# Optimization experiments

Measured on AMD Instinct MI355X. Metric: run time of the kernel, lower is better.

Reference implementation:

```python
import jax, jax.numpy as jnp
import numpy as np

EPS = 1e-6
NUM_HEADS = 16
CAPACITY_FACTOR = 0.5


def _layernorm(x, g, b):
    mu = jnp.mean(x, axis=-1, keepdims=True)
    var = jnp.mean((x - mu) ** 2, axis=-1, keepdims=True)
    return (x - mu) * jax.lax.rsqrt(var + EPS) * g + b


def setup_inputs() -> dict:
    key = jax.random.key(0)
    ks = jax.random.split(key, 12)
    B, S, H, F = 2, 2048, 1024, 4096
    s = lambda d: 1.0 / np.sqrt(d)
    return {
        "x": jax.random.normal(ks[0], (B, S, H), jnp.float32),
        "w_router": jax.random.normal(ks[1], (1, H), jnp.float32) * s(H),
        "ln1_g": jnp.ones((H,), jnp.float32),
        "ln1_b": jnp.zeros((H,), jnp.float32),
        "wq": jax.random.normal(ks[2], (H, H), jnp.float32) * s(H),
        "wk": jax.random.normal(ks[3], (H, H), jnp.float32) * s(H),
        "wv": jax.random.normal(ks[4], (H, H), jnp.float32) * s(H),
        "wo": jax.random.normal(ks[5], (H, H), jnp.float32) * s(H),
        "ln2_g": jnp.ones((H,), jnp.float32),
        "ln2_b": jnp.zeros((H,), jnp.float32),
        "w_gate": jax.random.normal(ks[6], (F, H), jnp.float32) * s(H),
        "w_up": jax.random.normal(ks[7], (F, H), jnp.float32) * s(H),
        "w_down": jax.random.normal(ks[8], (H, F), jnp.float32) * s(F),
    }


def reference(x, w_router, ln1_g, ln1_b, wq, wk, wv, wo, ln2_g, ln2_b, w_gate, w_up, w_down):
    B, S, H = x.shape
    nh = NUM_HEADS
    hd = H // nh
    scale = hd ** -0.5

    # --- TokenRouter (training path, straight-through) ---
    router_logits = jnp.einsum("bsh,oh->bso", x, w_router)[..., 0]  # [B,S]
    capacity = int(S * CAPACITY_FACTOR)
    _, top_idx = jax.lax.top_k(router_logits, capacity)  # [B,cap]
    routing_mask = jnp.zeros((B, S), x.dtype).at[jnp.arange(B)[:, None], top_idx].set(1.0)
    probs = jax.nn.sigmoid(router_logits)
    routing_weights = (routing_mask + probs - jax.lax.stop_gradient(probs))[..., None]  # [B,S,1]

    # --- Attention sub-block ---
    residual = x
    xn = _layernorm(x, ln1_g, ln1_b)
    q = jnp.einsum("bsh,oh->bso", xn, wq).reshape(B, S, nh, hd).transpose(0, 2, 1, 3)
    k = jnp.einsum("bsh,oh->bso", xn, wk).reshape(B, S, nh, hd).transpose(0, 2, 1, 3)
    v = jnp.einsum("bsh,oh->bso", xn, wv).reshape(B, S, nh, hd).transpose(0, 2, 1, 3)
    scores = jnp.einsum("bnqd,bnkd->bnqk", q, k) * scale
    causal = jnp.triu(jnp.full((S, S), -jnp.inf, x.dtype), k=1)
    attn = jax.nn.softmax(scores + causal, axis=-1)
    out = jnp.einsum("bnqk,bnkd->bnqd", attn, v).transpose(0, 2, 1, 3).reshape(B, S, H)
    attn_out = jnp.einsum("bsh,oh->bso", out, wo)
    x = residual + routing_weights * attn_out

    # --- FFN sub-block (SwiGLU) ---
    residual = x
    xn = _layernorm(x, ln2_g, ln2_b)
    gate = jax.nn.silu(jnp.einsum("bsh,fh->bsf", xn, w_gate))
    up = jnp.einsum("bsh,fh->bsf", xn, w_up)
    ffn_out = jnp.einsum("bsf,hf->bsh", gate * up, w_down)
    x = residual + routing_weights * ffn_out

    return x, router_logits
```

## Files before the change

### kernel.cpp

```cpp
#include <hip/hip_runtime.h>
#include <hip/hip_bf16.h>

typedef unsigned short u16;
typedef __attribute__((ext_vector_type(4))) float f32x4;
typedef __attribute__((ext_vector_type(8))) short short8;
typedef __attribute__((ext_vector_type(4))) unsigned short ushort4v;

__device__ __forceinline__ u16 f2bfu(float f) {
  unsigned int u = __float_as_uint(f);
  u += 0x7FFFu + ((u >> 16) & 1u);
  return (u16)(u >> 16);
}
__device__ __forceinline__ f32x4 mfma16(short8 a, short8 b, f32x4 c) {
  return __builtin_amdgcn_mfma_f32_16x16x32_bf16(a, b, c, 0, 0, 0);
}
__device__ __forceinline__ void gld16(const void* g, void* l) {
  __builtin_amdgcn_global_load_lds(
      (const __attribute__((address_space(1))) void*)g,
      (__attribute__((address_space(3))) void*)l, 16, 0, 0);
}

__global__ void k_cvt7(const float* __restrict__ s0, const float* __restrict__ s1,
                       const float* __restrict__ s2, const float* __restrict__ s3,
                       const float* __restrict__ s4, const float* __restrict__ s5,
                       const float* __restrict__ s6,
                       u16* __restrict__ d0, u16* __restrict__ d1, u16* __restrict__ d2,
                       u16* __restrict__ d3, u16* __restrict__ d4, u16* __restrict__ d5,
                       u16* __restrict__ d6) {
  const int y = blockIdx.y;
  const float* src; u16* dst; int n4;
  switch (y) {
    case 0: src = s0; dst = d0; n4 = 262144; break;
    case 1: src = s1; dst = d1; n4 = 262144; break;
    case 2: src = s2; dst = d2; n4 = 262144; break;
    case 3: src = s3; dst = d3; n4 = 262144; break;
    case 4: src = s4; dst = d4; n4 = 1048576; break;
    case 5: src = s5; dst = d5; n4 = 1048576; break;
    default: src = s6; dst = d6; n4 = 1048576; break;
  }
  int i = blockIdx.x * blockDim.x + threadIdx.x;
  if (i < n4) {
    float4 v = ((const float4*)src)[i];
    ushort4v o;
    o.x = f2bfu(v.x); o.y = f2bfu(v.y); o.z = f2bfu(v.z); o.w = f2bfu(v.w);
    *(ushort4v*)(dst + (size_t)i * 4) = o;
  }
}

__global__ void k_router(const float* __restrict__ x, const float* __restrict__ wr,
                         float* __restrict__ logits, float* __restrict__ out_lg,
                         float* __restrict__ out_x) {
  int t = blockIdx.x * 4 + (threadIdx.x >> 6);
  int l = threadIdx.x & 63;
  const float* xp = x + (size_t)t * 1024;
  float* op = out_x + (size_t)t * 1024;
  float s = 0.f;
#pragma unroll
  for (int p = 0; p < 4; ++p) {
    float4 xv = *(const float4*)(xp + (p * 64 + l) * 4);
    float4 wv = *(const float4*)(wr + (p * 64 + l) * 4);
    s += xv.x * wv.x + xv.y * wv.y + xv.z * wv.z + xv.w * wv.w;
    *(float4*)(op + (p * 64 + l) * 4) = xv;
  }
#pragma unroll
  for (int off = 32; off; off >>= 1) s += __shfl_xor(s, off);
  if (l == 0) { logits[t] = s; out_lg[t] = s; }
}

__global__ void k_mask(const float* __restrict__ logits, float* __restrict__ mask) {
  __shared__ float lg[2048];
  int b = blockIdx.y;
  const float* lp = logits + b * 2048;
  for (int j = threadIdx.x; j < 2048; j += 256) lg[j] = lp[j];
  __syncthreads();
  int t = threadIdx.x >> 2, qtr = threadIdx.x & 3;
  int i = blockIdx.x * 64 + t;
  float my = lg[i];
  int cnt = 0;
  for (int j = qtr * 512; j < qtr * 512 + 512; j += 4) {
    float4 v = *(const float4*)&lg[j];
    cnt += (v.x > my) || (v.x == my && (j + 0) < i);
    cnt += (v.y > my) || (v.y == my && (j + 1) < i);
    cnt += (v.z > my) || (v.z == my && (j + 2) < i);
    cnt += (v.w > my) || (v.w == my && (j + 3) < i);
  }
  cnt += __shfl_xor(cnt, 1);
  cnt += __shfl_xor(cnt, 2);
  if (qtr == 0) mask[b * 2048 + i] = (cnt < 1024) ? 1.0f : 0.0f;
}

__global__ void k_scan(const float* __restrict__ mask, int* __restrict__ idx) {
  __shared__ int wsum[4];
  int b = blockIdx.x;
  const float* mp = mask + b * 2048;
  int t = threadIdx.x, lane = t & 63, wv = t >> 6;
  int sel[8]; int c = 0;
#pragma unroll
  for (int j = 0; j < 8; ++j) { sel[j] = mp[t * 8 + j] > 0.5f; c += sel[j]; }
  int sc = c;
#pragma unroll
  for (int off = 1; off < 64; off <<= 1) {
    int u = __shfl_up(sc, off);
    if (lane >= off) sc += u;
  }
  if (lane == 63) wsum[wv] = sc;
  __syncthreads();
  int woff = 0;
  for (int i = 0; i < wv; ++i) woff += wsum[i];
  int pos = woff + sc - c;
#pragma unroll
  for (int j = 0; j < 8; ++j)
    if (sel[j]) idx[b * 1024 + pos++] = t * 8 + j;
}

__global__ void k_ln(const float* __restrict__ x, const float* __restrict__ g,
                     const float* __restrict__ bb, u16* __restrict__ out) {
  int t = blockIdx.x * 4 + (threadIdx.x >> 6);
  int l = threadIdx.x & 63;
  const float* xp = x + (size_t)t * 1024;
  float4 xv[4];
  float s = 0.f, sq = 0.f;
#pragma unroll
  for (int p = 0; p < 4; ++p) {
    xv[p] = *(const float4*)(xp + (p * 64 + l) * 4);
    s += xv[p].x + xv[p].y + xv[p].z + xv[p].w;
    sq += xv[p].x * xv[p].x + xv[p].y * xv[p].y + xv[p].z * xv[p].z + xv[p].w * xv[p].w;
  }
#pragma unroll
  for (int off = 32; off; off >>= 1) { s += __shfl_xor(s, off); sq += __shfl_xor(sq, off); }
  float mu = s * (1.f / 1024.f);
  float var = sq * (1.f / 1024.f) - mu * mu;
  float rs = rsqrtf(var + 1e-6f);
#pragma unroll
  for (int p = 0; p < 4; ++p) {
    float4 gv = *(const float4*)(g + (p * 64 + l) * 4);
    float4 bv = *(const float4*)(bb + (p * 64 + l) * 4);
    ushort4v o;
    o.x = f2bfu((xv[p].x - mu) * rs * gv.x + bv.x);
    o.y = f2bfu((xv[p].y - mu) * rs * gv.y + bv.y);
    o.z = f2bfu((xv[p].z - mu) * rs * gv.z + bv.z);
    o.w = f2bfu((xv[p].w - mu) * rs * gv.w + bv.w);
    *(ushort4v*)(out + (size_t)t * 1024 + (p * 64 + l) * 4) = o;
  }
}

__global__ void k_ln_g(const float* __restrict__ x, const int* __restrict__ idx,
                       const float* __restrict__ g, const float* __restrict__ bb,
                       u16* __restrict__ out) {
  int t = blockIdx.x * 4 + (threadIdx.x >> 6);
  int l = threadIdx.x & 63;
  int b = t >> 10;
  int orig = idx[b * 1024 + (t & 1023)];
  const float* xp = x + ((size_t)(b * 2048 + orig)) * 1024;
  float4 xv[4];
  float s = 0.f, sq = 0.f;
#pragma unroll
  for (int p = 0; p < 4; ++p) {
    xv[p] = *(const float4*)(xp + (p * 64 + l) * 4);
    s += xv[p].x + xv[p].y + xv[p].z + xv[p].w;
    sq += xv[p].x * xv[p].x + xv[p].y * xv[p].y + xv[p].z * xv[p].z + xv[p].w * xv[p].w;
  }
#pragma unroll
  for (int off = 32; off; off >>= 1) { s += __shfl_xor(s, off); sq += __shfl_xor(sq, off); }
  float mu = s * (1.f / 1024.f);
  float var = sq * (1.f / 1024.f) - mu * mu;
  float rs = rsqrtf(var + 1e-6f);
#pragma unroll
  for (int p = 0; p < 4; ++p) {
    float4 gv = *(const float4*)(g + (p * 64 + l) * 4);
    float4 bv = *(const float4*)(bb + (p * 64 + l) * 4);
    ushort4v o;
    o.x = f2bfu((xv[p].x - mu) * rs * gv.x + bv.x);
    o.y = f2bfu((xv[p].y - mu) * rs * gv.y + bv.y);
    o.z = f2bfu((xv[p].z - mu) * rs * gv.z + bv.z);
    o.w = f2bfu((xv[p].w - mu) * rs * gv.w + bv.w);
    *(ushort4v*)(out + (size_t)t * 1024 + (p * 64 + l) * 4) = o;
  }
}

__global__ void k_vtrans(const u16* __restrict__ V, u16* __restrict__ VT) {
  int bh = blockIdx.y;
  int b = bh >> 4, h = bh & 15;
  int w = threadIdx.x >> 6, l = threadIdx.x & 63;
  int s0 = (blockIdx.x * 4 + w) * 32;
  const u16* vb = V + ((size_t)b * 2048) * 1024 + h * 64 + l;
  u16 vals[32];
#pragma unroll
  for (int j = 0; j < 32; ++j) vals[j] = vb[(size_t)(s0 + j) * 1024];
  u16* ob = VT + ((size_t)bh * 64 + l) * 2048 + s0;
#pragma unroll
  for (int c = 0; c < 4; ++c) {
    short8 o;
#pragma unroll
    for (int j = 0; j < 8; ++j) o[j] = (short)vals[c * 8 + j];
    *(short8*)&ob[c * 8] = o;
  }
}

__device__ __forceinline__ void gemm_core64(
    const u16* __restrict__ A, const u16* __restrict__ W,
    u16 (&Al)[2][128][64], u16 (&Bl)[2][128][64],
    int m0, int n0, int K, int k0, int nsteps, f32x4 (&acc)[4][4]) {
  const int tid = threadIdx.x, w = tid >> 6, l = tid & 63;
  const int wr = (w >> 1) * 64, wc = (w & 1) * 64;
#pragma unroll
  for (int mt = 0; mt < 4; ++mt)
#pragma unroll
    for (int nt = 0; nt < 4; ++nt) acc[mt][nt] = (f32x4){0.f, 0.f, 0.f, 0.f};

  auto stage = [&](int bf, int t) {
#pragma unroll
    for (int i = 0; i < 4; ++i) {
      const int bc = (i * 4 + w) * 64;
      const int chunk = bc + l;
      const int row = chunk >> 3, cc = chunk & 7;
      gld16(A + (size_t)(m0 + row) * K + k0 + t * 64 + cc * 8, (char*)(&Al[bf][0][0]) + bc * 16);
      gld16(W + (size_t)(n0 + row) * K + k0 + t * 64 + cc * 8, (char*)(&Bl[bf][0][0]) + bc * 16);
    }
  };

  stage(0, 0);
  for (int t = 0; t < nsteps; ++t) {
    __syncthreads();
    if (t + 1 < nsteps) stage((t + 1) & 1, t + 1);
    const int bf = t & 1;
#pragma unroll
    for (int kk = 0; kk < 2; ++kk) {
      const int ko = kk * 32 + (l >> 4) * 8;
      short8 af[4], bv[4];
#pragma unroll
      for (int mt = 0; mt < 4; ++mt) af[mt] = *(const short8*)&Al[bf][wr + mt * 16 + (l & 15)][ko];
#pragma unroll
      for (int nt = 0; nt < 4; ++nt) bv[nt] = *(const short8*)&Bl[bf][wc + nt * 16 + (l & 15)][ko];
#pragma unroll
      for (int mt = 0; mt < 4; ++mt)
#pragma unroll
        for (int nt = 0; nt < 4; ++nt)
          acc[mt][nt] = mfma16(af[mt], bv[nt], acc[mt][nt]);
    }
  }
}

__global__ __launch_bounds__(256, 2)
void k_qkv(const u16* __restrict__ A,
           const u16* __restrict__ W0, const u16* __restrict__ W1, const u16* __restrict__ W2,
           u16* __restrict__ O0, u16* __restrict__ O1, u16* __restrict__ O2, int K) {
  __shared__ alignas(16) u16 Al[2][128][64];
  __shared__ alignas(16) u16 Bl[2][128][64];
  const int b = blockIdx.x, xcd = b & 7, k = b >> 3;
  const int rowg = xcd * 4 + k / 24, col = k % 24;
  const int sel = col >> 3;
  const u16* W = sel == 0 ? W0 : (sel == 1 ? W1 : W2);
  u16* Ot = sel == 0 ? O0 : (sel == 1 ? O1 : O2);
  const int n0 = (col & 7) * 128, m0 = rowg * 128;
  f32x4 acc[4][4];
  gemm_core64(A, W, Al, Bl, m0, n0, K, 0, K >> 6, acc);
  const int tid = threadIdx.x, w = tid >> 6, l = tid & 63;
  const int wr = (w >> 1) * 64, wc = (w & 1) * 64;
#pragma unroll
  for (int mt = 0; mt < 4; ++mt)
#pragma unroll
    for (int nt = 0; nt < 4; ++nt) {
      int row = m0 + wr + mt * 16 + ((l >> 4) << 2);
      int colo = n0 + wc + nt * 16 + (l & 15);
#pragma unroll
      for (int r = 0; r < 4; ++r)
        Ot[(size_t)(row + r) * 1024 + colo] = f2bfu(acc[mt][nt][r]);
    }
}

__global__ __launch_bounds__(256, 2)
void k_projsk(const u16* __restrict__ A, const u16* __restrict__ W,
              float* __restrict__ P0, float* __restrict__ P1,
              float* __restrict__ P2, float* __restrict__ P3,
              int K, int slice) {
  __shared__ alignas(16) u16 Al[2][128][64];
  __shared__ alignas(16) u16 Bl[2][128][64];
  const int b = blockIdx.x, xcd = b & 7, k = b >> 3;
  const int pair = xcd * 8 + (k >> 3);
  const int rowg = pair >> 2, z = pair & 3, col = k & 7;
  const int n0 = col * 128, m0 = rowg * 128, k0 = z * slice;
  float* P = z == 0 ? P0 : (z == 1 ? P1 : (z == 2 ? P2 : P3));
  f32x4 acc[4][4];
  gemm_core64(A, W, Al, Bl, m0, n0, K, k0, slice >> 6, acc);
  const int tid = threadIdx.x, w = tid >> 6, l = tid & 63;
  const int wr = (w >> 1) * 64, wc = (w & 1) * 64;
#pragma unroll
  for (int mt = 0; mt < 4; ++mt)
#pragma unroll
    for (int nt = 0; nt < 4; ++nt) {
      int row = m0 + wr + mt * 16 + ((l >> 4) << 2);
      int colo = n0 + wc + nt * 16 + (l & 15);
#pragma unroll
      for (int r = 0; r < 4; ++r)
        P[(size_t)(row + r) * 1024 + colo] = acc[mt][nt][r];
    }
}

__global__ void k_combine(const float* __restrict__ P0, const float* __restrict__ P1,
                          const float* __restrict__ P2, const float* __restrict__ P3,
                          const int* __restrict__ idx, const float* __restrict__ resid,
                          float* __restrict__ out) {
  int slot = blockIdx.x * 2 + (threadIdx.x >> 7);
  int c0 = (threadIdx.x & 127) * 8;
  int b = slot >> 10;
  int orig = idx[b * 1024 + (slot & 1023)];
  size_t po = (size_t)slot * 1024 + c0;
  size_t go = ((size_t)(b * 2048 + orig)) * 1024 + c0;
#pragma unroll
  for (int h = 0; h < 2; ++h) {
    float4 a = *(const float4*)(P0 + po + h * 4);
    float4 bb = *(const float4*)(P1 + po + h * 4);
    float4 c = *(const float4*)(P2 + po + h * 4);
    float4 d = *(const float4*)(P3 + po + h * 4);
    float4 rr = *(const float4*)(resid + go + h * 4);
    float4 o;
    o.x = rr.x + a.x + bb.x + c.x + d.x;
    o.y = rr.y + a.y + bb.y + c.y + d.y;
    o.z = rr.z + a.z + bb.z + c.z + d.z;
    o.w = rr.w + a.w + bb.w + c.w + d.w;
    *(float4*)(out + go + h * 4) = o;
  }
}

__global__ __launch_bounds__(256, 2)
void k_ffn_dual(const u16* __restrict__ A, const u16* __restrict__ Wg, const u16* __restrict__ Wu,
                u16* __restrict__ H, int N, int K) {
  __shared__ alignas(16) u16 Al[2][128][32];
  __shared__ alignas(16) u16 Bgl[2][128][32];
  __shared__ alignas(16) u16 Bul[2][128][32];
  const int tid = threadIdx.x, w = tid >> 6, l = tid & 63;
  const int b = blockIdx.x, xcd = b & 7, k = b >> 3;
  const int rowg = xcd * 2 + (k >> 5), col = k & 31;
  const int n0 = col * 128, m0 = rowg * 128;
  const int wr = (w >> 1) * 64, wc = (w & 1) * 64;
  f32x4 ag[4][4], au[4][4];
#pragma unroll
  for (int mt = 0; mt < 4; ++mt)
#pragma unroll
    for (int nt = 0; nt < 4; ++nt) {
      ag[mt][nt] = (f32x4){0.f, 0.f, 0.f, 0.f};
      au[mt][nt] = (f32x4){0.f, 0.f, 0.f, 0.f};
    }
  const int nsteps = K >> 5;

  auto stage = [&](int bf, int t) {
#pragma unroll
    for (int i = 0; i < 2; ++i) {
      const int bc = (i * 4 + w) * 64;
      const int chunk = bc + l;
      const int row = chunk >> 2, cc = chunk & 3;
      const size_t ao = (size_t)(m0 + row) * K + t * 32 + cc * 8;
      const size_t bo = (size_t)(n0 + row) * K + t * 32 + cc * 8;
      gld16(A + ao,  (char*)(&Al[bf][0][0])  + bc * 16);
      gld16(Wg + bo, (char*)(&Bgl[bf][0][0]) + bc * 16);
      gld16(Wu + bo, (char*)(&Bul[bf][0][0]) + bc * 16);
    }
  };

  stage(0, 0);
  for (int t = 0; t < nsteps; ++t) {
    __syncthreads();
    if (t + 1 < nsteps) stage((t + 1) & 1, t + 1);
    const int bf = t & 1;
    const int ko = (l >> 4) * 8;
    short8 af[4], bg[4], bu[4];
#pragma unroll
    for (int mt = 0; mt < 4; ++mt) af[mt] = *(const short8*)&Al[bf][wr + mt * 16 + (l & 15)][ko];
#pragma unroll
    for (int nt = 0; nt < 4; ++nt) {
      bg[nt] = *(const short8*)&Bgl[bf][wc + nt * 16 + (l & 15)][ko];
      bu[nt] = *(const short8*)&Bul[bf][wc + nt * 16 + (l & 15)][ko];
    }
#pragma unroll
    for (int mt = 0; mt < 4; ++mt)
#pragma unroll
      for (int nt = 0; nt < 4; ++nt) {
        ag[mt][nt] = mfma16(af[mt], bg[nt], ag[mt][nt]);
        au[mt][nt] = mfma16(af[mt], bu[nt], au[mt][nt]);
      }
  }
#pragma unroll
  for (int mt = 0; mt < 4; ++mt)
#pragma unroll
    for (int nt = 0; nt < 4; ++nt) {
      int row = m0 + wr + mt * 16 + ((l >> 4) << 2);
      int col2 = n0 + wc + nt * 16 + (l & 15);
#pragma unroll
      for (int r = 0; r < 4; ++r) {
        float g = ag[mt][nt][r], u = au[mt][nt][r];
        float sg = g / (1.f + __expf(-g));
        H[(size_t)(row + r) * N + col2] = f2bfu(sg * u);
      }
    }
}

__global__ __launch_bounds__(512, 4)
void k_attn(const u16* __restrict__ Q, const u16* __restrict__ K,
            const u16* __restrict__ VT, const int* __restrict__ idx,
            u16* __restrict__ O) {
  const int S = 2048, HH = 1024;
  const int px = blockIdx.x, bh = blockIdx.y;
  const int b = bh >> 4, h = bh & 15;
  const int tid = threadIdx.x;
  const int g = tid >> 8;
  const int tg = tid & 255;
  const int w = tg >> 6;
  const int l = tid & 63;
  __shared__ alignas(16) u16 Kl[2][64][72];
  __shared__ alignas(16) u16 Vtl[2][64][72];
  __shared__ alignas(16) u16 Pl[8][16][72];
  __shared__ alignas(16) float cm[4][64][24];
  const size_t base = ((size_t)b * S) * HH + h * 64;
  const u16* vtb = VT + ((size_t)bh * 64) * S;
  const int* ib = idx + b * 1024;

  const int r0 = tg >> 3,          cc0 = (tg & 7) * 8;
  const int r1 = (256 + tg) >> 3,  cc1 = (tg & 7) * 8;

  auto flash = [&](int qt) {
    const int slot0 = qt * 64 + w * 16 + ((l >> 4) << 2);
    const int slotA = qt * 64 + w * 16 + (l & 15);
    const int qrowA = ib[slotA];
    int qp[4];
#pragma unroll
    for (int r = 0; r < 4; ++r) qp[r] = ib[slot0 + r];
    const int nkt = (ib[qt * 64 + 63] >> 6) + 1;
    const int hh = (nkt + 1) >> 1;
    const int kt_base = g ? hh : 0;
    const int kt_end  = g ? nkt : hh;

    short8 qf[2];
#pragma unroll
    for (int kk = 0; kk < 2; ++kk)
      qf[kk] = *(const short8*)&Q[base + (size_t)qrowA * HH + kk * 32 + (l >> 4) * 8];

    f32x4 accO[4];
    float m[4], ls[4];
#pragma unroll
    for (int dt = 0; dt < 4; ++dt) accO[dt] = (f32x4){0.f, 0.f, 0.f, 0.f};
#pragma unroll
    for (int r = 0; r < 4; ++r) { m[r] = -1e30f; ls[r] = 0.f; }

    short8 kreg0, kreg1, vreg0, vreg1;
    auto loadregs = [&](int kt) {
      kreg0 = *(const short8*)&K[base + (size_t)(kt * 64 + r0) * HH + cc0];
      kreg1 = *(const short8*)&K[base + (size_t)(kt * 64 + r1) * HH + cc1];
      vreg0 = *(const short8*)&vtb[(size_t)r0 * S + kt * 64 + cc0];
      vreg1 = *(const short8*)&vtb[(size_t)r1 * S + kt * 64 + cc1];
    };
    if (kt_base < kt_end) loadregs(kt_base);

    for (int i = 0; i < hh; ++i) {
      const int kt = kt_base + i;
      const bool valid = kt < kt_end;
      __syncthreads();
      if (valid) {
        *(short8*)&Kl[g][r0][cc0]  = kreg0;
        *(short8*)&Kl[g][r1][cc1]  = kreg1;
        *(short8*)&Vtl[g][r0][cc0] = vreg0;
        *(short8*)&Vtl[g][r1][cc1] = vreg1;
        if (kt + 1 < kt_end) loadregs(kt + 1);
      }
      __syncthreads();
      if (!valid) continue;

      float p[4][4];
      const int kcb = kt * 64 + (l & 15);
#pragma unroll
      for (int ct = 0; ct < 4; ++ct) {
        f32x4 a = (f32x4){0.f, 0.f, 0.f, 0.f};
#pragma unroll
        for (int kk = 0; kk < 2; ++kk) {
          short8 kf = *(const short8*)&Kl[g][ct * 16 + (l & 15)][kk * 32 + (l >> 4) * 8];
          a = mfma16(qf[kk], kf, a);
        }
#pragma unroll
        for (int r = 0; r < 4; ++r) {
          float v = a[r] * 0.125f;
          if ((kcb + ct * 16) > qp[r]) v = -1e30f;
          p[ct][r] = v;
        }
      }
#pragma unroll
      for (int r = 0; r < 4; ++r) {
        float mx = fmaxf(fmaxf(p[0][r], p[1][r]), fmaxf(p[2][r], p[3][r]));
#pragma unroll
        for (int off = 1; off < 16; off <<= 1) mx = fmaxf(mx, __shfl_xor(mx, off));
        float mn = fmaxf(m[r], mx);
        float alpha = __expf(m[r] - mn);
        m[r] = mn;
        float ps = 0.f;
#pragma unroll
        for (int ct = 0; ct < 4; ++ct) { float e = __expf(p[ct][r] - mn); p[ct][r] = e; ps += e; }
#pragma unroll
        for (int off = 1; off < 16; off <<= 1) ps += __shfl_xor(ps, off);
        ls[r] = ls[r] * alpha + ps;
#pragma unroll
        for (int dt = 0; dt < 4; ++dt) accO[dt][r] *= alpha;
      }
#pragma unroll
      for (int ct = 0; ct < 4; ++ct)
#pragma unroll
        for (int r = 0; r < 4; ++r)
          Pl[g * 4 + w][((l >> 4) << 2) + r][ct * 16 + (l & 15)] = f2bfu(p[ct][r]);
      short8 pa[2];
#pragma unroll
      for (int kk = 0; kk < 2; ++kk)
        pa[kk] = *(const short8*)&Pl[g * 4 + w][l & 15][kk * 32 + (l >> 4) * 8];
#pragma unroll
      for (int dt = 0; dt < 4; ++dt)
#pragma unroll
        for (int kk = 0; kk < 2; ++kk) {
          short8 vf = *(const short8*)&Vtl[g][dt * 16 + (l & 15)][kk * 32 + (l >> 4) * 8];
          accO[dt] = mfma16(pa[kk], vf, accO[dt]);
        }
    }

    __syncthreads();
    if (g == 1) {
      float* dst = &cm[w][l][0];
#pragma unroll
      for (int r = 0; r < 4; ++r) { dst[r] = m[r]; dst[4 + r] = ls[r]; }
#pragma unroll
      for (int dt = 0; dt < 4; ++dt)
#pragma unroll
        for (int r = 0; r < 4; ++r) dst[8 + dt * 4 + r] = accO[dt][r];
    }
    __syncthreads();
    if (g == 0) {
      const float* src = &cm[w][l][0];
#pragma unroll
      for (int r = 0; r < 4; ++r) {
        float m1 = src[r], ls1 = src[4 + r];
        float mm = fmaxf(m[r], m1);
        float a0 = __expf(m[r] - mm), a1 = __expf(m1 - mm);
        float lsf = ls[r] * a0 + ls1 * a1;
        float inv = 1.f / lsf;
#pragma unroll
        for (int dt = 0; dt < 4; ++dt) {
          float v = (accO[dt][r] * a0 + src[8 + dt * 4 + r] * a1) * inv;
          O[((size_t)(b * 1024 + slot0 + r)) * HH + h * 64 + dt * 16 + (l & 15)] = f2bfu(v);
        }
      }
    }
  };

  flash(px);
  flash(15 - px);
}

extern "C" void kernel_launch(void* const* d_in, const int* in_sizes, int n_in,
                              void* d_out, int out_size, void* d_ws, size_t ws_size,
                              hipStream_t stream) {
  const float* x  = (const float*)d_in[0];
  const float* wr = (const float*)d_in[1];
  const float* g1 = (const float*)d_in[2];
  const float* b1 = (const float*)d_in[3];
  const float* wq = (const float*)d_in[4];
  const float* wk = (const float*)d_in[5];
  const float* wv = (const float*)d_in[6];
  const float* wo = (const float*)d_in[7];
  const float* g2 = (const float*)d_in[8];
  const float* b2 = (const float*)d_in[9];
  const float* wg = (const float*)d_in[10];
  const float* wu = (const float*)d_in[11];
  const float* wd = (const float*)d_in[12];

  float* out_x  = (float*)d_out;
  float* out_lg = out_x + (size_t)4096 * 1024;

  char* p = (char*)d_ws;
  float* mask   = (float*)p;             p += 16384;
  float* logits = (float*)p;             p += 16384;
  int*   idx    = (int*)p;               p += 16384;
  u16* wq_b = (u16*)p;                   p += (size_t)1048576 * 2;
  u16* wk_b = (u16*)p;                   p += (size_t)1048576 * 2;
  u16* wv_b = (u16*)p;                   p += (size_t)1048576 * 2;
  u16* wo_b = (u16*)p;                   p += (size_t)1048576 * 2;
  u16* wg_b = (u16*)p;                   p += (size_t)4194304 * 2;
  u16* wu_b = (u16*)p;                   p += (size_t)4194304 * 2;
  u16* wd_b = (u16*)p;                   p += (size_t)4194304 * 2;
  u16* xn   = (u16*)p;                   p += (size_t)4194304 * 2;
  u16* q_b  = (u16*)p;                   p += (size_t)4194304 * 2;
  u16* k_b  = (u16*)p;                   p += (size_t)4194304 * 2;
  u16* v_b  = (u16*)p;                   p += (size_t)4194304 * 2;
  u16* ao_b = (u16*)p;                   p += (size_t)2097152 * 2;
  u16* vt_b = (u16*)p;                   p += (size_t)4194304 * 2;
  float* pextra = (float*)p;             p += (size_t)2097152 * 4;
  u16* h_b  = q_b;

  float* oP0 = (float*)xn;  float* oP1 = (float*)v_b;
  float* oP2 = (float*)q_b; float* oP3 = (float*)k_b;
  float* dP0 = (float*)xn;  float* dP1 = (float*)v_b;
  float* dP2 = (float*)vt_b; float* dP3 = pextra;

  k_cvt7<<<dim3(4096, 7), 256, 0, stream>>>(wq, wk, wv, wo, wg, wu, wd,
                                            wq_b, wk_b, wv_b, wo_b, wg_b, wu_b, wd_b);

  k_router<<<1024, 256, 0, stream>>>(x, wr, logits, out_lg, out_x);
  k_mask<<<dim3(32, 2), 256, 0, stream>>>(logits, mask);
  k_scan<<<2, 256, 0, stream>>>(mask, idx);

  k_ln<<<1024, 256, 0, stream>>>(x, g1, b1, xn);
  k_qkv<<<768, 256, 0, stream>>>(xn, wq_b, wk_b, wv_b, q_b, k_b, v_b, 1024);
  k_vtrans<<<dim3(16, 32), 256, 0, stream>>>(v_b, vt_b);
  k_attn<<<dim3(8, 32), 512, 0, stream>>>(q_b, k_b, vt_b, idx, ao_b);
  k_projsk<<<512, 256, 0, stream>>>(ao_b, wo_b, oP0, oP1, oP2, oP3, 1024, 256);
  k_combine<<<1024, 256, 0, stream>>>(oP0, oP1, oP2, oP3, idx, x, out_x);

  k_ln_g<<<512, 256, 0, stream>>>(out_x, idx, g2, b2, xn);
  k_ffn_dual<<<512, 256, 0, stream>>>(xn, wg_b, wu_b, h_b, 4096, 1024);
  k_projsk<<<512, 256, 0, stream>>>(h_b, wd_b, dP0, dP1, dP2, dP3, 4096, 1024);
  k_combine<<<1024, 256, 0, stream>>>(dP0, dP1, dP2, dP3, idx, out_x, out_x);
}
```

Baseline: 260.2 us.

## Fuse router with LayerNorm and compute Q only for routed tokens

```diff
diff --git a/kernel.cpp b/kernel.cpp
--- a/kernel.cpp
+++ b/kernel.cpp
@@ -47,24 +47,46 @@
   }
 }
 
-__global__ void k_router(const float* __restrict__ x, const float* __restrict__ wr,
-                         float* __restrict__ logits, float* __restrict__ out_lg,
-                         float* __restrict__ out_x) {
+__global__ void k_router_ln(const float* __restrict__ x, const float* __restrict__ wr,
+                            const float* __restrict__ g, const float* __restrict__ bb,
+                            float* __restrict__ logits, float* __restrict__ out_lg,
+                            float* __restrict__ out_x, u16* __restrict__ xn) {
   int t = blockIdx.x * 4 + (threadIdx.x >> 6);
   int l = threadIdx.x & 63;
   const float* xp = x + (size_t)t * 1024;
   float* op = out_x + (size_t)t * 1024;
-  float s = 0.f;
+  float4 xv[4];
+  float s = 0.f, sq = 0.f, lg = 0.f;
 #pragma unroll
   for (int p = 0; p < 4; ++p) {
-    float4 xv = *(const float4*)(xp + (p * 64 + l) * 4);
+    xv[p] = *(const float4*)(xp + (p * 64 + l) * 4);
     float4 wv = *(const float4*)(wr + (p * 64 + l) * 4);
-    s += xv.x * wv.x + xv.y * wv.y + xv.z * wv.z + xv.w * wv.w;
-    *(float4*)(op + (p * 64 + l) * 4) = xv;
-  }
-#pragma unroll
-  for (int off = 32; off; off >>= 1) s += __shfl_xor(s, off);
-  if (l == 0) { logits[t] = s; out_lg[t] = s; }
+    lg += xv[p].x * wv.x + xv[p].y * wv.y + xv[p].z * wv.z + xv[p].w * wv.w;
+    s += xv[p].x + xv[p].y + xv[p].z + xv[p].w;
+    sq += xv[p].x * xv[p].x + xv[p].y * xv[p].y + xv[p].z * xv[p].z + xv[p].w * xv[p].w;
+    *(float4*)(op + (p * 64 + l) * 4) = xv[p];
+  }
+#pragma unroll
+  for (int off = 32; off; off >>= 1) {
+    lg += __shfl_xor(lg, off);
+    s += __shfl_xor(s, off);
+    sq += __shfl_xor(sq, off);
+  }
+  float mu = s * (1.f / 1024.f);
+  float var = sq * (1.f / 1024.f) - mu * mu;
+  float rs = rsqrtf(var + 1e-6f);
+#pragma unroll
+  for (int p = 0; p < 4; ++p) {
+    float4 gv = *(const float4*)(g + (p * 64 + l) * 4);
+    float4 bv = *(const float4*)(bb + (p * 64 + l) * 4);
+    ushort4v o;
+    o.x = f2bfu((xv[p].x - mu) * rs * gv.x + bv.x);
+    o.y = f2bfu((xv[p].y - mu) * rs * gv.y + bv.y);
+    o.z = f2bfu((xv[p].z - mu) * rs * gv.z + bv.z);
+    o.w = f2bfu((xv[p].w - mu) * rs * gv.w + bv.w);
+    *(ushort4v*)(xn + (size_t)t * 1024 + (p * 64 + l) * 4) = o;
+  }
+  if (l == 0) { logits[t] = lg; out_lg[t] = lg; }
 }
 
 __global__ void k_mask(const float* __restrict__ logits, float* __restrict__ mask) {
@@ -113,37 +135,6 @@
     if (sel[j]) idx[b * 1024 + pos++] = t * 8 + j;
 }
 
-__global__ void k_ln(const float* __restrict__ x, const float* __restrict__ g,
-                     const float* __restrict__ bb, u16* __restrict__ out) {
-  int t = blockIdx.x * 4 + (threadIdx.x >> 6);
-  int l = threadIdx.x & 63;
-  const float* xp = x + (size_t)t * 1024;
-  float4 xv[4];
-  float s = 0.f, sq = 0.f;
-#pragma unroll
-  for (int p = 0; p < 4; ++p) {
-    xv[p] = *(const float4*)(xp + (p * 64 + l) * 4);
-    s += xv[p].x + xv[p].y + xv[p].z + xv[p].w;
-    sq += xv[p].x * xv[p].x + xv[p].y * xv[p].y + xv[p].z * xv[p].z + xv[p].w * xv[p].w;
-  }
-#pragma unroll
-  for (int off = 32; off; off >>= 1) { s += __shfl_xor(s, off); sq += __shfl_xor(sq, off); }
-  float mu = s * (1.f / 1024.f);
-  float var = sq * (1.f / 1024.f) - mu * mu;
-  float rs = rsqrtf(var + 1e-6f);
-#pragma unroll
-  for (int p = 0; p < 4; ++p) {
-    float4 gv = *(const float4*)(g + (p * 64 + l) * 4);
-    float4 bv = *(const float4*)(bb + (p * 64 + l) * 4);
-    ushort4v o;
-    o.x = f2bfu((xv[p].x - mu) * rs * gv.x + bv.x);
-    o.y = f2bfu((xv[p].y - mu) * rs * gv.y + bv.y);
-    o.z = f2bfu((xv[p].z - mu) * rs * gv.z + bv.z);
-    o.w = f2bfu((xv[p].w - mu) * rs * gv.w + bv.w);
-    *(ushort4v*)(out + (size_t)t * 1024 + (p * 64 + l) * 4) = o;
-  }
-}
-
 __global__ void k_ln_g(const float* __restrict__ x, const int* __restrict__ idx,
                        const float* __restrict__ g, const float* __restrict__ bb,
                        u16* __restrict__ out) {
@@ -242,21 +233,75 @@
 }
 
 __global__ __launch_bounds__(256, 2)
-void k_qkv(const u16* __restrict__ A,
-           const u16* __restrict__ W0, const u16* __restrict__ W1, const u16* __restrict__ W2,
-           u16* __restrict__ O0, u16* __restrict__ O1, u16* __restrict__ O2, int K) {
+void k_qkv2(const u16* __restrict__ A, const int* __restrict__ idx,
+            const u16* __restrict__ Wq, const u16* __restrict__ Wk, const u16* __restrict__ Wv,
+            u16* __restrict__ Qc, u16* __restrict__ Ko, u16* __restrict__ Vo) {
   __shared__ alignas(16) u16 Al[2][128][64];
   __shared__ alignas(16) u16 Bl[2][128][64];
-  const int b = blockIdx.x, xcd = b & 7, k = b >> 3;
-  const int rowg = xcd * 4 + k / 24, col = k % 24;
-  const int sel = col >> 3;
-  const u16* W = sel == 0 ? W0 : (sel == 1 ? W1 : W2);
-  u16* Ot = sel == 0 ? O0 : (sel == 1 ? O1 : O2);
-  const int n0 = (col & 7) * 128, m0 = rowg * 128;
+  const int tid = threadIdx.x, w = tid >> 6, l = tid & 63;
+  const int b = blockIdx.x, xcd = b & 7, j = b >> 3;
+  const u16* W; u16* Ot; int m0, n0; bool isQ;
+  if (j < 16) {
+    isQ = true;
+    int rowg = (xcd >> 1) * 4 + (j >> 2);
+    int col  = (xcd & 1) * 4 + (j & 3);
+    m0 = rowg * 128; n0 = col * 128; W = Wq; Ot = Qc;
+  } else {
+    isQ = false;
+    int jj = j - 16;
+    int rowg = (xcd >> 1) * 8 + (jj >> 3);
+    int colg = (xcd & 1) * 8 + (jj & 7);
+    m0 = rowg * 128; n0 = (colg & 7) * 128;
+    W = (colg >> 3) ? Wv : Wk; Ot = (colg >> 3) ? Vo : Ko;
+  }
+  int srow[4];
+#pragma unroll
+  for (int i = 0; i < 4; ++i) {
+    int r = (((i * 4 + w) * 64) + l) >> 3;
+    int row = m0 + r;
+    if (isQ) {
+      int b2 = row >> 10;
+      srow[i] = b2 * 2048 + idx[b2 * 1024 + (row & 1023)];
+    } else srow[i] = row;
+  }
+  const int wr = (w >> 1) * 64, wc = (w & 1) * 64;
   f32x4 acc[4][4];
-  gemm_core64(A, W, Al, Bl, m0, n0, K, 0, K >> 6, acc);
-  const int tid = threadIdx.x, w = tid >> 6, l = tid & 63;
-  const int wr = (w >> 1) * 64, wc = (w & 1) * 64;
+#pragma unroll
+  for (int mt = 0; mt < 4; ++mt)
+#pragma unroll
+    for (int nt = 0; nt < 4; ++nt) acc[mt][nt] = (f32x4){0.f, 0.f, 0.f, 0.f};
+
+  auto stage = [&](int bf, int t) {
+#pragma unroll
+    for (int i = 0; i < 4; ++i) {
+      const int bc = (i * 4 + w) * 64;
+      const int chunk = bc + l;
+      const int r = chunk >> 3, cc = chunk & 7;
+      gld16(A + (size_t)srow[i] * 1024 + t * 64 + cc * 8, (char*)(&Al[bf][0][0]) + bc * 16);
+      gld16(W + (size_t)(n0 + r) * 1024 + t * 64 + cc * 8, (char*)(&Bl[bf][0][0]) + bc * 16);
+    }
+  };
+
+  stage(0, 0);
+  for (int t = 0; t < 16; ++t) {
+    __syncthreads();
+    if (t + 1 < 16) stage((t + 1) & 1, t + 1);
+    const int bf = t & 1;
+#pragma unroll
+    for (int kk = 0; kk < 2; ++kk) {
+      const int ko = kk * 32 + (l >> 4) * 8;
+      short8 af[4], bv[4];
+#pragma unroll
+      for (int mt = 0; mt < 4; ++mt) af[mt] = *(const short8*)&Al[bf][wr + mt * 16 + (l & 15)][ko];
+#pragma unroll
+      for (int nt = 0; nt < 4; ++nt) bv[nt] = *(const short8*)&Bl[bf][wc + nt * 16 + (l & 15)][ko];
+#pragma unroll
+      for (int mt = 0; mt < 4; ++mt)
+#pragma unroll
+        for (int nt = 0; nt < 4; ++nt)
+          acc[mt][nt] = mfma16(af[mt], bv[nt], acc[mt][nt]);
+    }
+  }
 #pragma unroll
   for (int mt = 0; mt < 4; ++mt)
 #pragma unroll
@@ -412,6 +457,7 @@
   __shared__ alignas(16) u16 Pl[8][16][72];
   __shared__ alignas(16) float cm[4][64][24];
   const size_t base = ((size_t)b * S) * HH + h * 64;
+  const size_t qbase = ((size_t)b * 1024) * HH + h * 64;
   const u16* vtb = VT + ((size_t)bh * 64) * S;
   const int* ib = idx + b * 1024;
 
@@ -421,7 +467,6 @@
   auto flash = [&](int qt) {
     const int slot0 = qt * 64 + w * 16 + ((l >> 4) << 2);
     const int slotA = qt * 64 + w * 16 + (l & 15);
-    const int qrowA = ib[slotA];
     int qp[4];
 #pragma unroll
     for (int r = 0; r < 4; ++r) qp[r] = ib[slot0 + r];
@@ -433,7 +478,7 @@
     short8 qf[2];
 #pragma unroll
     for (int kk = 0; kk < 2; ++kk)
-      qf[kk] = *(const short8*)&Q[base + (size_t)qrowA * HH + kk * 32 + (l >> 4) * 8];
+      qf[kk] = *(const short8*)&Q[qbase + (size_t)slotA * HH + kk * 32 + (l >> 4) * 8];
 
     f32x4 accO[4];
     float m[4], ls[4];
@@ -598,12 +643,11 @@
   k_cvt7<<<dim3(4096, 7), 256, 0, stream>>>(wq, wk, wv, wo, wg, wu, wd,
                                             wq_b, wk_b, wv_b, wo_b, wg_b, wu_b, wd_b);
 
-  k_router<<<1024, 256, 0, stream>>>(x, wr, logits, out_lg, out_x);
+  k_router_ln<<<1024, 256, 0, stream>>>(x, wr, g1, b1, logits, out_lg, out_x, xn);
   k_mask<<<dim3(32, 2), 256, 0, stream>>>(logits, mask);
   k_scan<<<2, 256, 0, stream>>>(mask, idx);
 
-  k_ln<<<1024, 256, 0, stream>>>(x, g1, b1, xn);
-  k_qkv<<<768, 256, 0, stream>>>(xn, wq_b, wk_b, wv_b, q_b, k_b, v_b, 1024);
+  k_qkv2<<<640, 256, 0, stream>>>(xn, idx, wq_b, wk_b, wv_b, q_b, k_b, v_b);
   k_vtrans<<<dim3(16, 32), 256, 0, stream>>>(v_b, vt_b);
   k_attn<<<dim3(8, 32), 512, 0, stream>>>(q_b, k_b, vt_b, idx, ao_b);
   k_projsk<<<512, 256, 0, stream>>>(ao_b, wo_b, oP0, oP1, oP2, oP3, 1024, 256);
```

Result: no change. 258.2 us (-0.8%).
